# Kernel optimization log

Hardware: AMD Instinct MI355X
Metric: run time of the kernel (lower is better)

The kernel has to match this reference:

```python
import jax, jax.numpy as jnp
import numpy as np

RELU_SCALE = 0.25  # const power-of-two activation scale for QuantReLU (uint4)
DN = ('NCHW', 'OIHW', 'NCHW')
BN_EPS = 1e-5


def ste_round(x):
    # straight-through-estimator round (brevitas RoundSte)
    return x + jax.lax.stop_gradient(jnp.round(x) - x)


def fq_signed(x, bits):
    # per-tensor symmetric fixed-point fake quant with power-of-two scale
    # (Int8WeightPerTensorFixedPoint / Int8ActPerTensorFixedPoint at bit_width=bits)
    n = 2.0 ** (bits - 1) - 1.0
    m = jnp.maximum(jnp.max(jnp.abs(x)), 1e-8)
    s = jax.lax.stop_gradient(jnp.exp2(jnp.ceil(jnp.log2(m / n))))
    return jnp.clip(ste_round(x / s), -n - 1.0, n) * s


def quant_relu4(x):
    # QuantReLU: uint4, CONST power-of-two scale
    return jnp.clip(ste_round(x / RELU_SCALE), 0.0, 15.0) * RELU_SCALE


def bn(x, g, b, m, v):
    # inference-form BatchNorm2d (running stats)
    inv = g * jax.lax.rsqrt(v + BN_EPS)
    return x * inv[None, :, None, None] + (b - m * inv)[None, :, None, None]


def qconv(x, w, stride, groups):
    # QuantConv2d: fake-quant input (int4) and weight (int4), then conv
    xq = fq_signed(x, 4)
    wq = fq_signed(w, 4)
    pad = 'VALID' if w.shape[-1] == 1 else ((1, 1), (1, 1))
    return jax.lax.conv_general_dilated(
        xq, wq, (stride, stride), pad,
        dimension_numbers=DN, feature_group_count=groups)


def setup_inputs() -> dict:
    key = jax.random.key(0)
    ks = jax.random.split(key, 24)
    B, Cin, H, W = 32, 64, 56, 56
    expansion, Cout = 6, 96
    P = expansion * Cin  # 384

    def bn_params(i, C):
        g = jax.random.uniform(ks[i], (C,), minval=0.5, maxval=1.5)
        b = jax.random.normal(ks[i + 1], (C,)) * 0.1
        m = jax.random.normal(ks[i + 2], (C,)) * 0.1
        v = jax.random.uniform(ks[i + 3], (C,), minval=0.5, maxval=1.5)
        return g, b, m, v

    x = jax.random.normal(ks[0], (B, Cin, H, W), dtype=jnp.float32)
    w1 = jax.random.normal(ks[1], (P, Cin, 1, 1), dtype=jnp.float32) * 0.1
    w2 = jax.random.normal(ks[2], (P, 1, 3, 3), dtype=jnp.float32) * 0.1
    w3 = jax.random.normal(ks[3], (Cout, P, 1, 1), dtype=jnp.float32) * 0.1
    ws = jax.random.normal(ks[4], (Cout, Cin, 1, 1), dtype=jnp.float32) * 0.1
    g1, b1, m1, v1 = bn_params(5, P)
    g2, b2, m2, v2 = bn_params(9, P)
    g3, b3, m3, v3 = bn_params(13, Cout)
    gs, bs, ms, vs = bn_params(17, Cout)
    return {
        'x': x,
        'w1': w1, 'g1': g1, 'b1': b1, 'm1': m1, 'v1': v1,
        'w2': w2, 'g2': g2, 'b2': b2, 'm2': m2, 'v2': v2,
        'w3': w3, 'g3': g3, 'b3': b3, 'm3': m3, 'v3': v3,
        'ws': ws, 'gs': gs, 'bs': bs, 'ms': ms, 'vs': vs,
    }


def reference(x, w1, g1, b1, m1, v1, w2, g2, b2, m2, v2,
              w3, g3, b3, m3, v3, ws, gs, bs, ms, vs):
    P = w1.shape[0]
    # expand 1x1 -> BN -> QuantReLU
    out = quant_relu4(bn(qconv(x, w1, 1, 1), g1, b1, m1, v1))
    # depthwise 3x3 (stride=1) -> BN -> QuantReLU
    out = quant_relu4(bn(qconv(out, w2, 1, P), g2, b2, m2, v2))
    # project 1x1 with int8 output_quant -> BN
    out = bn(fq_signed(qconv(out, w3, 1, 1), 8), g3, b3, m3, v3)
    # shortcut: 1x1 quant conv (int4 output_quant) -> BN  (stride==1, Cin!=Cout)
    sc = bn(fq_signed(qconv(x, ws, 1, 1), 4), gs, bs, ms, vs)
    return quant_relu4(out + sc)
```

## Files before the change

### kernel.cpp

```cpp
#include <hip/hip_runtime.h>
#include <stdint.h>

#define B_  32
#define CIN 64
#define H_  56
#define W_  56
#define HW_ 3136
#define P_  384
#define CO_ 96

__device__ __forceinline__ float pot_scale(float m, float n) {
    float q = fmaxf(m, 1e-8f) / n;
    int e; float f = frexpf(q, &e);
    return ldexpf(1.0f, (f == 0.5f) ? (e - 1) : e);
}

__device__ __forceinline__ int dot8(int a, int b, int c) {
#if __has_builtin(__builtin_amdgcn_sdot8)
    return __builtin_amdgcn_sdot8(a, b, c, false);
#else
#pragma unroll
    for (int j = 0; j < 8; j++) {
        int av = (a << (28 - 4 * j)) >> 28;
        int bv = (b << (28 - 4 * j)) >> 28;
        c += av * bv;
    }
    return c;
#endif
}

__device__ __forceinline__ int iclamp(int v, int lo, int hi) { return min(max(v, lo), hi); }

__device__ __forceinline__ unsigned build_lut(float r, int lo) {
    unsigned v = 0;
#pragma unroll
    for (int L = 0; L < 8; L++)
        v |= (unsigned)min((int)rintf(__fmul_rn((float)(lo + L), r)), 7) << (4 * L);
    return v;
}
__device__ __forceinline__ int lut1(unsigned lo, unsigned hi, int L) {
    unsigned sel = (L & 8) ? hi : lo;
    return (int)((sel >> ((L & 7) * 4)) & 7u);
}
__device__ __forceinline__ unsigned lutn4(unsigned lo, unsigned hi, unsigned v) {
    return (unsigned)lut1(lo, hi, (int)(v & 0xffu))
         | ((unsigned)lut1(lo, hi, (int)((v >> 8) & 0xffu)) << 4)
         | ((unsigned)lut1(lo, hi, (int)((v >> 16) & 0xffu)) << 8)
         | ((unsigned)lut1(lo, hi, (int)((v >> 24) & 0xffu)) << 12);
}

__device__ __forceinline__ int block_max(int v, int* red) {
    int tid = threadIdx.x;
    red[tid] = v; __syncthreads();
    for (int s = 128; s > 0; s >>= 1) {
        if (tid < s) red[tid] = max(red[tid], red[tid + s]);
        __syncthreads();
    }
    int r = red[0];
    __syncthreads();
    return r;
}

__device__ __forceinline__ int block_max192(int v, int* red) {
    int tid = threadIdx.x;
    red[tid] = v;
    if (tid < 64) red[192 + tid] = 0;
    __syncthreads();
    for (int s = 128; s > 0; s >>= 1) {
        if (tid < s) red[tid] = max(red[tid], red[tid + s]);
        __syncthreads();
    }
    int r = red[0];
    __syncthreads();
    return r;
}


__global__ __launch_bounds__(1024) void k_init_bn(
    float* sf, float* bnb,
    const float* g1, const float* b1, const float* m1, const float* v1,
    const float* g2, const float* b2, const float* m2, const float* v2,
    const float* g3, const float* b3, const float* m3, const float* v3,
    const float* gs, const float* bs, const float* ms, const float* vs)
{
    int t = threadIdx.x;
    if (t < 32) ((int*)sf)[t] = 0;
    if (t < 384) {
        float inv = __fmul_rn(g1[t], __fdiv_rn(1.0f, sqrtf(__fadd_rn(v1[t], 1e-5f))));
        bnb[t] = inv;
        bnb[384 + t] = __fsub_rn(b1[t], __fmul_rn(m1[t], inv));
    } else if (t < 768) {
        int i = t - 384;
        float inv = __fmul_rn(g2[i], __fdiv_rn(1.0f, sqrtf(__fadd_rn(v2[i], 1e-5f))));
        bnb[768 + i] = inv;
        bnb[1152 + i] = __fsub_rn(b2[i], __fmul_rn(m2[i], inv));
    } else if (t < 864) {
        int i = t - 768;
        float inv = __fmul_rn(g3[i], __fdiv_rn(1.0f, sqrtf(__fadd_rn(v3[i], 1e-5f))));
        bnb[1536 + i] = inv;
        bnb[1632 + i] = __fsub_rn(b3[i], __fmul_rn(m3[i], inv));
    } else if (t < 960) {
        int i = t - 864;
        float inv = __fmul_rn(gs[i], __fdiv_rn(1.0f, sqrtf(__fadd_rn(vs[i], 1e-5f))));
        bnb[1728 + i] = inv;
        bnb[1824 + i] = __fsub_rn(bs[i], __fmul_rn(ms[i], inv));
    }
}

#define XBLK 2044
__global__ __launch_bounds__(256) void k_maxes(
    const float* __restrict__ x, const float* __restrict__ w1,
    const float* __restrict__ w2, const float* __restrict__ w3,
    const float* __restrict__ wsc, float* sf)
{
    __shared__ int red[256];
    int tid = threadIdx.x;
    float m = 0.f;
    if (blockIdx.x < XBLK) {
        const float4* x4 = (const float4*)x;
        const int n4 = (B_ * CIN * HW_) / 4;
        for (int i = blockIdx.x * 256 + tid; i < n4; i += XBLK * 256) {
            float4 v = x4[i];
            m = fmaxf(m, fmaxf(fmaxf(fabsf(v.x), fabsf(v.y)),
                               fmaxf(fabsf(v.z), fabsf(v.w))));
        }
        int bm = block_max(__float_as_int(m), red);
        if (tid == 0) atomicMax((int*)&sf[0], bm);
    } else {
        int seg = blockIdx.x - XBLK;
        const float* p = seg == 0 ? w1 : seg == 1 ? w2 : seg == 2 ? w3 : wsc;
        int n = seg == 0 ? P_ * CIN : seg == 1 ? P_ * 9 : seg == 2 ? CO_ * P_ : CO_ * CIN;
        for (int i = tid; i < n; i += 256) m = fmaxf(m, fabsf(p[i]));
        int bm = block_max(__float_as_int(m), red);
        if (tid == 0) atomicMax((int*)&sf[1 + seg], bm);
    }
}

__global__ __launch_bounds__(256) void k_quantx(
    const float* __restrict__ x, const float* __restrict__ sf, int* __restrict__ xq4)
{
    int t = blockIdx.x * 256 + threadIdx.x;
    float rx = 1.0f / pot_scale(sf[0], 7.0f);
    int hw4 = (t % 784) * 4;
    int c8  = (t / 784) & 7;
    int b   = t / (784 * 8);
    const float* xp = x + (size_t)(b * 64 + c8 * 8) * HW_ + hw4;
    unsigned pk[4] = {0, 0, 0, 0};
#pragma unroll
    for (int j = 0; j < 8; j++) {
        float4 v = *(const float4*)(xp + (size_t)j * HW_);
        float va[4] = {v.x, v.y, v.z, v.w};
#pragma unroll
        for (int w = 0; w < 4; w++) {
            int q = iclamp((int)rintf(__fmul_rn(va[w], rx)), -8, 7);
            pk[w] |= (unsigned)(q & 0xF) << (4 * j);
        }
    }
    int4 st = make_int4((int)pk[0], (int)pk[1], (int)pk[2], (int)pk[3]);
    *(int4*)(xq4 + (size_t)(b * 8 + c8) * HW_ + hw4) = st;
}

__global__ __launch_bounds__(256) void k_quantw(
    const float* __restrict__ w1, const float* __restrict__ w2,
    const float* __restrict__ w3, const float* __restrict__ wsc,
    const float* __restrict__ sf,
    int* __restrict__ w1n, int8_t* __restrict__ w2q,
    int* __restrict__ w3n, int* __restrict__ wsn)
{
    int flat = blockIdx.x * 256 + threadIdx.x;
    if (flat < 3072) {
        int d = flat, co = d & 3, k8 = (d >> 2) & 7, g = d >> 5;
        float r = 1.0f / pot_scale(sf[1], 7.f);
        const float* src = w1 + (4 * g + co) * 64 + 8 * k8;
        unsigned pk = 0;
#pragma unroll
        for (int j = 0; j < 8; j++) {
            int q = iclamp((int)rintf(__fmul_rn(src[j], r)), -8, 7);
            pk |= (unsigned)(q & 0xF) << (4 * j);
        }
        w1n[d] = (int)pk;
    } else if (flat < 7680) {
        int d = flat - 3072, co = d & 3, k8 = (d >> 2) % 48, coq = d / 192;
        float r = 1.0f / pot_scale(sf[3], 7.f);
        const float* src = w3 + (4 * coq + co) * 384 + 8 * k8;
        unsigned pk = 0;
#pragma unroll
        for (int j = 0; j < 8; j++) {
            int q = iclamp((int)rintf(__fmul_rn(src[j], r)), -8, 7);
            pk |= (unsigned)(q & 0xF) << (4 * j);
        }
        w3n[d] = (int)pk;
    } else if (flat < 8448) {
        int d = flat - 7680, co = d & 3, k8 = (d >> 2) & 7, coq = d >> 5;
        float r = 1.0f / pot_scale(sf[4], 7.f);
        const float* src = wsc + (4 * coq + co) * 64 + 8 * k8;
        unsigned pk = 0;
#pragma unroll
        for (int j = 0; j < 8; j++) {
            int q = iclamp((int)rintf(__fmul_rn(src[j], r)), -8, 7);
            pk |= (unsigned)(q & 0xF) << (4 * j);
        }
        wsn[d] = (int)pk;
    } else if (flat < 11904) {
        int i = flat - 8448;
        float r = 1.0f / pot_scale(sf[2], 7.f);
        w2q[i] = (int8_t)iclamp((int)rintf(__fmul_rn(w2[i], r)), -8, 7);
    }
}

__global__ __launch_bounds__(192) void k_conv1(
    const int* __restrict__ xq4, const int4* __restrict__ w1n,
    const int4* __restrict__ wsn,
    const float* __restrict__ sf, const float* __restrict__ bnb,
    unsigned* __restrict__ out1p, int* si)
{
    __shared__ __align__(16) int xs[8 * W_];
    __shared__ int red[256];
    int tid = threadIdx.x;
    int b = blockIdx.x / H_, h = blockIdx.x % H_;
    for (int i = tid; i < 8 * W_; i += 192)
        xs[i] = xq4[((b * 8 + i / W_) * HW_) + h * W_ + (i % W_)];
    float sprod = __fmul_rn(pot_scale(sf[0], 7.f), pot_scale(sf[1], 7.f));
    __syncthreads();
    int g = tid % 96, half = tid / 96;
    int4 wreg[8];
    {
        const int4* wp = w1n + g * 8;
#pragma unroll
        for (int k = 0; k < 8; k++) wreg[k] = wp[k];
    }
    float4 invv = *(const float4*)&bnb[4 * g];
    float4 betv = *(const float4*)&bnb[384 + 4 * g];
    float inva[4] = {invv.x, invv.y, invv.z, invv.w};
    float beta[4] = {betv.x, betv.y, betv.z, betv.w};
    int lmax = 0;
    unsigned* dst = out1p + (size_t)(b * 96 + g) * HW_ + h * W_;
#pragma unroll
    for (int q = 0; q < 7; q++) {
        int w4 = half * 28 + q * 4;
        int acc[4][4];
#pragma unroll
        for (int c = 0; c < 4; c++)
#pragma unroll
            for (int w = 0; w < 4; w++) acc[c][w] = 0;
#pragma unroll
        for (int k = 0; k < 8; k++) {
            int4 wv = wreg[k];
            int4 xv = *(const int4*)&xs[k * W_ + w4];
            acc[0][0] = dot8(xv.x, wv.x, acc[0][0]); acc[0][1] = dot8(xv.y, wv.x, acc[0][1]);
            acc[0][2] = dot8(xv.z, wv.x, acc[0][2]); acc[0][3] = dot8(xv.w, wv.x, acc[0][3]);
            acc[1][0] = dot8(xv.x, wv.y, acc[1][0]); acc[1][1] = dot8(xv.y, wv.y, acc[1][1]);
            acc[1][2] = dot8(xv.z, wv.y, acc[1][2]); acc[1][3] = dot8(xv.w, wv.y, acc[1][3]);
            acc[2][0] = dot8(xv.x, wv.z, acc[2][0]); acc[2][1] = dot8(xv.y, wv.z, acc[2][1]);
            acc[2][2] = dot8(xv.z, wv.z, acc[2][2]); acc[2][3] = dot8(xv.w, wv.z, acc[2][3]);
            acc[3][0] = dot8(xv.x, wv.w, acc[3][0]); acc[3][1] = dot8(xv.y, wv.w, acc[3][1]);
            acc[3][2] = dot8(xv.z, wv.w, acc[3][2]); acc[3][3] = dot8(xv.w, wv.w, acc[3][3]);
        }
        uint4 ov;
        unsigned* op = (unsigned*)&ov;
#pragma unroll
        for (int w = 0; w < 4; w++) {
            unsigned pkd = 0;
#pragma unroll
            for (int c = 0; c < 4; c++) {
                float y = __fadd_rn(__fmul_rn(__fmul_rn((float)acc[c][w], sprod), inva[c]), beta[c]);
                int L = iclamp((int)rintf(__fmul_rn(y, 4.f)), 0, 15);
                lmax = max(lmax, L);
                pkd |= (unsigned)L << (8 * c);
            }
            op[w] = pkd;
        }
        *(uint4*)(dst + w4) = ov;
    }
    int bm = block_max192(lmax, red);
    if (tid == 0) atomicMax(&si[5], bm);
    int amax = 0;
    for (int qi = tid; qi < 336; qi += 192) {
        int coq = qi / 14, w4 = (qi % 14) * 4;
        int acc[4][4];
#pragma unroll
        for (int c = 0; c < 4; c++)
#pragma unroll
            for (int w = 0; w < 4; w++) acc[c][w] = 0;
        const int4* wp = wsn + coq * 8;
#pragma unroll
        for (int k = 0; k < 8; k++) {
            int4 wv = wp[k];
            int4 xv = *(const int4*)&xs[k * W_ + w4];
            acc[0][0] = dot8(xv.x, wv.x, acc[0][0]); acc[0][1] = dot8(xv.y, wv.x, acc[0][1]);
            acc[0][2] = dot8(xv.z, wv.x, acc[0][2]); acc[0][3] = dot8(xv.w, wv.x, acc[0][3]);
            acc[1][0] = dot8(xv.x, wv.y, acc[1][0]); acc[1][1] = dot8(xv.y, wv.y, acc[1][1]);
            acc[1][2] = dot8(xv.z, wv.y, acc[1][2]); acc[1][3] = dot8(xv.w, wv.y, acc[1][3]);
            acc[2][0] = dot8(xv.x, wv.z, acc[2][0]); acc[2][1] = dot8(xv.y, wv.z, acc[2][1]);
            acc[2][2] = dot8(xv.z, wv.z, acc[2][2]); acc[2][3] = dot8(xv.w, wv.z, acc[2][3]);
            acc[3][0] = dot8(xv.x, wv.w, acc[3][0]); acc[3][1] = dot8(xv.y, wv.w, acc[3][1]);
            acc[3][2] = dot8(xv.z, wv.w, acc[3][2]); acc[3][3] = dot8(xv.w, wv.w, acc[3][3]);
        }
#pragma unroll
        for (int c = 0; c < 4; c++)
            amax = max(amax, max(max(abs(acc[c][0]), abs(acc[c][1])),
                                 max(abs(acc[c][2]), abs(acc[c][3]))));
    }
    bm = block_max192(amax, red);
    if (tid == 0) atomicMax(&si[8], bm);
}

__global__ __launch_bounds__(256) void k_conv2(
    const unsigned* __restrict__ out1p, const int8_t* __restrict__ w2q,
    const float* __restrict__ sf, int* si,
    const float* __restrict__ bnb, unsigned* __restrict__ out2p)
{
    __shared__ int plane[58 * 58];
    __shared__ int red[256];
    int tid = threadIdx.x;
    int b = blockIdx.x / 96, g = blockIdx.x % 96;
    float s_a2 = pot_scale(0.25f * (float)si[5], 7.f);
    float r2 = 0.25f / s_a2;
    float sprod = __fmul_rn(s_a2, pot_scale(sf[2], 7.f));
    unsigned lutlo = build_lut(r2, 0), luthi = build_lut(r2, 8);
    const unsigned* src = out1p + (size_t)(b * 96 + g) * HW_;
    for (int i = tid; i < 58 * 58; i += 256) {
        int r = i / 58, c = i % 58;
        int pv = 0;
        if (r >= 1 && r <= 56 && c >= 1 && c <= 56) {
            unsigned v = src[(r - 1) * W_ + (c - 1)];
            pv = lut1(lutlo, luthi, (int)(v & 0xffu))
               | (lut1(lutlo, luthi, (int)((v >> 8) & 0xffu)) << 8)
               | (lut1(lutlo, luthi, (int)((v >> 16) & 0xffu)) << 16)
               | (lut1(lutlo, luthi, (int)((v >> 24) & 0xffu)) << 24);
        }
        plane[i] = pv;
    }
    int wv[4][9];
#pragma unroll
    for (int c = 0; c < 4; c++)
#pragma unroll
        for (int t = 0; t < 9; t++) wv[c][t] = (int)w2q[(4 * g + c) * 9 + t];
    float4 invv = *(const float4*)&bnb[768 + 4 * g];
    float4 betv = *(const float4*)&bnb[1152 + 4 * g];
    float inva[4] = {invv.x, invv.y, invv.z, invv.w};
    float beta[4] = {betv.x, betv.y, betv.z, betv.w};
    __syncthreads();
    int lmax = 0;
    int ow = tid & 63, seg = tid >> 6;
    if (ow < 56) {
        int oh0 = seg * 14;
        const int* pr = plane + ow;
        unsigned* dst = out2p + (size_t)(b * 96 + g) * HW_ + ow;
        int p00 = pr[oh0 * 58],       p01 = pr[oh0 * 58 + 1],       p02 = pr[oh0 * 58 + 2];
        int p10 = pr[(oh0 + 1) * 58], p11 = pr[(oh0 + 1) * 58 + 1], p12 = pr[(oh0 + 1) * 58 + 2];
#pragma unroll 2
        for (int oh = oh0; oh < oh0 + 14; oh++) {
            int p20 = pr[(oh + 2) * 58], p21 = pr[(oh + 2) * 58 + 1], p22 = pr[(oh + 2) * 58 + 2];
            unsigned pkd = 0;
#pragma unroll
            for (int c = 0; c < 4; c++) {
                int sh = 8 * c;
                int acc = ((p00 >> sh) & 0xff) * wv[c][0] + ((p01 >> sh) & 0xff) * wv[c][1]
                        + ((p02 >> sh) & 0xff) * wv[c][2] + ((p10 >> sh) & 0xff) * wv[c][3]
                        + ((p11 >> sh) & 0xff) * wv[c][4] + ((p12 >> sh) & 0xff) * wv[c][5]
                        + ((p20 >> sh) & 0xff) * wv[c][6] + ((p21 >> sh) & 0xff) * wv[c][7]
                        + ((p22 >> sh) & 0xff) * wv[c][8];
                float y = __fadd_rn(__fmul_rn(__fmul_rn((float)acc, sprod), inva[c]), beta[c]);
                int L = iclamp((int)rintf(__fmul_rn(y, 4.f)), 0, 15);
                lmax = max(lmax, L);
                pkd |= (unsigned)L << sh;
            }
            dst[oh * W_] = pkd;
            p00 = p10; p01 = p11; p02 = p12;
            p10 = p20; p11 = p21; p12 = p22;
        }
    }
    int bm = block_max(lmax, red);
    if (tid == 0) atomicMax(&si[6], bm);
}

__global__ __launch_bounds__(256) void k_conv3(
    const unsigned* __restrict__ out2p, const int4* __restrict__ w3n,
    const float* __restrict__ sf, int* si,
    int16_t* __restrict__ acc3)
{
    __shared__ __align__(16) int a3s[2 * 48 * W_];
    __shared__ int red[256];
    int tid = threadIdx.x;
    int b = blockIdx.x / 28, h0 = (blockIdx.x % 28) * 2;
    float s_a3 = pot_scale(0.25f * (float)si[6], 7.f);
    float r3 = 0.25f / s_a3;
    unsigned lutlo = build_lut(r3, 0), luthi = build_lut(r3, 8);
    for (int i = tid; i < 2 * 48 * W_; i += 256) {
        int row = i / (48 * W_), rem = i % (48 * W_), c8 = rem / W_, w = rem % W_;
        size_t base = (size_t)(b * 96 + c8 * 2) * HW_ + (h0 + row) * W_ + w;
        unsigned v0 = out2p[base], v1 = out2p[base + HW_];
        a3s[i] = (int)(lutn4(lutlo, luthi, v0) | (lutn4(lutlo, luthi, v1) << 16));
    }
    __syncthreads();
    int amax = 0;
    for (int qi = tid; qi < 672; qi += 256) {
        int coq = qi / 28, rem2 = qi % 28, row = rem2 / 14, w4 = (rem2 % 14) * 4;
        int acc[4][4];
#pragma unroll
        for (int c = 0; c < 4; c++)
#pragma unroll
            for (int w = 0; w < 4; w++) acc[c][w] = 0;
        const int4* wp = w3n + coq * 48;
        const int* ap = a3s + row * 48 * W_ + w4;
#pragma unroll 6
        for (int k = 0; k < 48; k++) {
            int4 wv = wp[k];
            int4 av = *(const int4*)(ap + k * W_);
            acc[0][0] = dot8(av.x, wv.x, acc[0][0]); acc[0][1] = dot8(av.y, wv.x, acc[0][1]);
            acc[0][2] = dot8(av.z, wv.x, acc[0][2]); acc[0][3] = dot8(av.w, wv.x, acc[0][3]);
            acc[1][0] = dot8(av.x, wv.y, acc[1][0]); acc[1][1] = dot8(av.y, wv.y, acc[1][1]);
            acc[1][2] = dot8(av.z, wv.y, acc[1][2]); acc[1][3] = dot8(av.w, wv.y, acc[1][3]);
            acc[2][0] = dot8(av.x, wv.z, acc[2][0]); acc[2][1] = dot8(av.y, wv.z, acc[2][1]);
            acc[2][2] = dot8(av.z, wv.z, acc[2][2]); acc[2][3] = dot8(av.w, wv.z, acc[2][3]);
            acc[3][0] = dot8(av.x, wv.w, acc[3][0]); acc[3][1] = dot8(av.y, wv.w, acc[3][1]);
            acc[3][2] = dot8(av.z, wv.w, acc[3][2]); acc[3][3] = dot8(av.w, wv.w, acc[3][3]);
        }
#pragma unroll
        for (int c = 0; c < 4; c++) {
            int co = coq * 4 + c;
            amax = max(amax, max(max(abs(acc[c][0]), abs(acc[c][1])),
                                 max(abs(acc[c][2]), abs(acc[c][3]))));
            short4 st = make_short4((short)acc[c][0], (short)acc[c][1],
                                    (short)acc[c][2], (short)acc[c][3]);
            *(short4*)(acc3 + (size_t)(b * CO_ + co) * HW_ + (h0 + row) * W_ + w4) = st;
        }
    }
    int bm = block_max(amax, red);
    if (tid == 0) atomicMax(&si[7], bm);
}

__global__ __launch_bounds__(256) void k_final(
    const int* __restrict__ xq4, const int4* __restrict__ wsn,
    const int16_t* __restrict__ acc3, const float* __restrict__ sf,
    const int* __restrict__ si, const float* __restrict__ bnb,
    float* __restrict__ dout)
{
    __shared__ __align__(16) int xs[8 * W_];
    int tid = threadIdx.x;
    int b = blockIdx.x / H_, h = blockIdx.x % H_;
    for (int i = tid; i < 8 * W_; i += 256)
        xs[i] = xq4[((b * 8 + i / W_) * HW_) + h * W_ + (i % W_)];
    float s_a3   = pot_scale(0.25f * (float)si[6], 7.f);
    float sprod3 = __fmul_rn(s_a3, pot_scale(sf[3], 7.f));
    float s_q3   = pot_scale(__fmul_rn(sprod3, (float)si[7]), 127.f);
    float rq3    = sprod3 / s_q3;
    float sprods = __fmul_rn(pot_scale(sf[0], 7.f), pot_scale(sf[4], 7.f));
    float s_qs   = pot_scale(__fmul_rn(sprods, (float)si[8]), 7.f);
    float rqs    = sprods / s_qs;
    __syncthreads();
    for (int qi = tid; qi < 24 * 14; qi += 256) {
        int coq = qi / 14, w4 = (qi % 14) * 4;
        int acc[4][4];
#pragma unroll
        for (int c = 0; c < 4; c++)
#pragma unroll
            for (int w = 0; w < 4; w++) acc[c][w] = 0;
        const int4* wp = wsn + coq * 8;
#pragma unroll
        for (int k = 0; k < 8; k++) {
            int4 wv = wp[k];
            int4 xv = *(const int4*)&xs[k * W_ + w4];
            acc[0][0] = dot8(xv.x, wv.x, acc[0][0]); acc[0][1] = dot8(xv.y, wv.x, acc[0][1]);
            acc[0][2] = dot8(xv.z, wv.x, acc[0][2]); acc[0][3] = dot8(xv.w, wv.x, acc[0][3]);
            acc[1][0] = dot8(xv.x, wv.y, acc[1][0]); acc[1][1] = dot8(xv.y, wv.y, acc[1][1]);
            acc[1][2] = dot8(xv.z, wv.y, acc[1][2]); acc[1][3] = dot8(xv.w, wv.y, acc[1][3]);
            acc[2][0] = dot8(xv.x, wv.z, acc[2][0]); acc[2][1] = dot8(xv.y, wv.z, acc[2][1]);
            acc[2][2] = dot8(xv.z, wv.z, acc[2][2]); acc[2][3] = dot8(xv.w, wv.z, acc[2][3]);
            acc[3][0] = dot8(xv.x, wv.w, acc[3][0]); acc[3][1] = dot8(xv.y, wv.w, acc[3][1]);
            acc[3][2] = dot8(xv.z, wv.w, acc[3][2]); acc[3][3] = dot8(xv.w, wv.w, acc[3][3]);
        }
        float4 inv3v = *(const float4*)&bnb[1536 + 4 * coq];
        float4 bet3v = *(const float4*)&bnb[1632 + 4 * coq];
        float4 invSv = *(const float4*)&bnb[1728 + 4 * coq];
        float4 betSv = *(const float4*)&bnb[1824 + 4 * coq];
        float inv3a[4] = {inv3v.x, inv3v.y, inv3v.z, inv3v.w};
        float bet3a[4] = {bet3v.x, bet3v.y, bet3v.z, bet3v.w};
        float invSa[4] = {invSv.x, invSv.y, invSv.z, invSv.w};
        float betSa[4] = {betSv.x, betSv.y, betSv.z, betSv.w};
#pragma unroll
        for (int c = 0; c < 4; c++) {
            int co = coq * 4 + c;
            size_t idx = (size_t)(b * CO_ + co) * HW_ + h * W_ + w4;
            short4 c3 = *(const short4*)(acc3 + idx);
            int c3a[4] = {c3.x, c3.y, c3.z, c3.w};
            float4 o4;
            float* o = (float*)&o4;
#pragma unroll
            for (int j = 0; j < 4; j++) {
                int q3 = iclamp((int)rintf(__fmul_rn((float)c3a[j], rq3)), -128, 127);
                float y3 = __fadd_rn(__fmul_rn(__fmul_rn((float)q3, s_q3), inv3a[c]), bet3a[c]);
                int qs = iclamp((int)rintf(__fmul_rn((float)acc[c][j], rqs)), -8, 7);
                float ys = __fadd_rn(__fmul_rn(__fmul_rn((float)qs, s_qs), invSa[c]), betSa[c]);
                float oo = __fadd_rn(y3, ys);
                int L = iclamp((int)rintf(__fmul_rn(oo, 4.f)), 0, 15);
                o[j] = (float)L * 0.25f;
            }
            *(float4*)(dout + idx) = o4;
        }
    }
}

extern "C" void kernel_launch(void* const* d_in, const int* in_sizes, int n_in,
                              void* d_out, int out_size, void* d_ws, size_t ws_size,
                              hipStream_t stream)
{
    const float* x   = (const float*)d_in[0];
    const float* w1  = (const float*)d_in[1];
    const float* g1  = (const float*)d_in[2];
    const float* b1  = (const float*)d_in[3];
    const float* m1  = (const float*)d_in[4];
    const float* v1  = (const float*)d_in[5];
    const float* w2  = (const float*)d_in[6];
    const float* g2  = (const float*)d_in[7];
    const float* b2  = (const float*)d_in[8];
    const float* m2  = (const float*)d_in[9];
    const float* v2  = (const float*)d_in[10];
    const float* w3  = (const float*)d_in[11];
    const float* g3  = (const float*)d_in[12];
    const float* b3  = (const float*)d_in[13];
    const float* m3  = (const float*)d_in[14];
    const float* v3  = (const float*)d_in[15];
    const float* wsc = (const float*)d_in[16];
    const float* gs  = (const float*)d_in[17];
    const float* bs  = (const float*)d_in[18];
    const float* ms  = (const float*)d_in[19];
    const float* vs  = (const float*)d_in[20];

    char* ws = (char*)d_ws;
    float*    sf    = (float*)ws;
    int*      si    = (int*)ws;
    float*    bnb   = (float*)(ws + 256);
    int*      w1n   = (int*)(ws + 8192);
    int8_t*   w2q   = (int8_t*)(ws + 32768);
    int*      w3n   = (int*)(ws + 36864);
    int*      wsn   = (int*)(ws + 73728);
    int*      xq4   = (int*)(ws + (1u << 20));
    unsigned* out1p = (unsigned*)(ws + (8u << 20));
    int16_t*  acc3  = (int16_t*)(ws + (8u << 20));
    unsigned* out2p = (unsigned*)(ws + (48u << 20));

    k_init_bn<<<1, 1024, 0, stream>>>(sf, bnb, g1, b1, m1, v1, g2, b2, m2, v2,
                                      g3, b3, m3, v3, gs, bs, ms, vs);
    k_maxes<<<XBLK + 4, 256, 0, stream>>>(x, w1, w2, w3, wsc, sf);
    k_quantx<<<784, 256, 0, stream>>>(x, sf, xq4);
    k_quantw<<<47, 256, 0, stream>>>(w1, w2, w3, wsc, sf, w1n, w2q, w3n, wsn);
    k_conv1<<<B_ * H_, 192, 0, stream>>>(xq4, (const int4*)w1n, (const int4*)wsn,
                                         sf, bnb, out1p, si);
    k_conv2<<<B_ * 96, 256, 0, stream>>>(out1p, w2q, sf, si, bnb, out2p);
    k_conv3<<<B_ * 28, 256, 0, stream>>>(out2p, (const int4*)w3n, sf, si, acc3);
    k_final<<<B_ * H_, 256, 0, stream>>>(xq4, (const int4*)wsn, acc3, sf, si, bnb,
                                         (float*)d_out);
}
```

Baseline: 313.9 us.

## Fuse input quantization into conv1, pack activations to 4-bit, spread max atomics

Removes the separate k_quantx pass: conv1 now quantizes x rows on the fly and writes xq4 as a side output for the final kernel. Intermediate activations out1/out2 go from one byte per 4-bit level to 16-bit nibble-packed storage, halving their write and read traffic, and conv1 stages its output in shared memory so it can store with wide coalesced writes. Block reductions switch to wave shuffles, and the global max atomics go to 16 padded slots that readers combine, to cut atomic contention. The x max scan also uses fewer blocks. The cost is that conv1 does strided float loads of x itself and every consumer reads 16 slots per max.

Measured after the change: 274.4 us. 1.14x faster.

```diff
diff --git a/kernel.cpp b/kernel.cpp
--- a/kernel.cpp
+++ b/kernel.cpp
@@ -9,6 +9,8 @@
 #define P_  384
 #define CO_ 96
 
+typedef unsigned short u16;
+
 __device__ __forceinline__ float pot_scale(float m, float n) {
     float q = fmaxf(m, 1e-8f) / n;
     int e; float f = frexpf(q, &e);
@@ -42,42 +44,34 @@
     unsigned sel = (L & 8) ? hi : lo;
     return (int)((sel >> ((L & 7) * 4)) & 7u);
 }
-__device__ __forceinline__ unsigned lutn4(unsigned lo, unsigned hi, unsigned v) {
-    return (unsigned)lut1(lo, hi, (int)(v & 0xffu))
-         | ((unsigned)lut1(lo, hi, (int)((v >> 8) & 0xffu)) << 4)
-         | ((unsigned)lut1(lo, hi, (int)((v >> 16) & 0xffu)) << 8)
-         | ((unsigned)lut1(lo, hi, (int)((v >> 24) & 0xffu)) << 12);
-}
-
-__device__ __forceinline__ int block_max(int v, int* red) {
-    int tid = threadIdx.x;
-    red[tid] = v; __syncthreads();
-    for (int s = 128; s > 0; s >>= 1) {
-        if (tid < s) red[tid] = max(red[tid], red[tid + s]);
-        __syncthreads();
-    }
-    int r = red[0];
+__device__ __forceinline__ unsigned lutn4h(unsigned lo, unsigned hi, unsigned v) {
+    return (unsigned)lut1(lo, hi, (int)(v & 0xFu))
+         | ((unsigned)lut1(lo, hi, (int)((v >> 4) & 0xFu)) << 4)
+         | ((unsigned)lut1(lo, hi, (int)((v >> 8) & 0xFu)) << 8)
+         | ((unsigned)lut1(lo, hi, (int)((v >> 12) & 0xFu)) << 12);
+}
+
+__device__ __forceinline__ int wave_max(int v) {
+#pragma unroll
+    for (int off = 32; off > 0; off >>= 1) v = max(v, __shfl_xor(v, off, 64));
+    return v;
+}
+__device__ __forceinline__ int block_max_w(int v, int* red, int slot, int nw) {
+    v = wave_max(v);
+    int wid = threadIdx.x >> 6;
+    if ((threadIdx.x & 63) == 0) red[slot * 8 + wid] = v;
     __syncthreads();
+    int r = red[slot * 8];
+#pragma unroll 4
+    for (int i = 1; i < nw; i++) r = max(r, red[slot * 8 + i]);
     return r;
 }
 
-__device__ __forceinline__ int block_max192(int v, int* red) {
-    int tid = threadIdx.x;
-    red[tid] = v;
-    if (tid < 64) red[192 + tid] = 0;
-    __syncthreads();
-    for (int s = 128; s > 0; s >>= 1) {
-        if (tid < s) red[tid] = max(red[tid], red[tid + s]);
-        __syncthreads();
-    }
-    int r = red[0];
-    __syncthreads();
-    return r;
-}
-
+#define SMAX_RD(sm, q, dst) { dst = 0; _Pragma("unroll") \
+    for (int s_ = 0; s_ < 16; s_++) dst = max(dst, (sm)[(q) * 256 + s_ * 16]); }
 
 __global__ __launch_bounds__(1024) void k_init_bn(
-    float* sf, float* bnb,
+    float* sf, int* smax, float* bnb,
     const float* g1, const float* b1, const float* m1, const float* v1,
     const float* g2, const float* b2, const float* m2, const float* v2,
     const float* g3, const float* b3, const float* m3, const float* v3,
@@ -85,6 +79,7 @@
 {
     int t = threadIdx.x;
     if (t < 32) ((int*)sf)[t] = 0;
+    smax[t] = 0;
     if (t < 384) {
         float inv = __fmul_rn(g1[t], __fdiv_rn(1.0f, sqrtf(__fadd_rn(v1[t], 1e-5f))));
         bnb[t] = inv;
@@ -107,13 +102,13 @@
     }
 }
 
-#define XBLK 2044
+#define XBLK 384
 __global__ __launch_bounds__(256) void k_maxes(
     const float* __restrict__ x, const float* __restrict__ w1,
     const float* __restrict__ w2, const float* __restrict__ w3,
     const float* __restrict__ wsc, float* sf)
 {
-    __shared__ int red[256];
+    __shared__ int red[16];
     int tid = threadIdx.x;
     float m = 0.f;
     if (blockIdx.x < XBLK) {
@@ -124,40 +119,16 @@
             m = fmaxf(m, fmaxf(fmaxf(fabsf(v.x), fabsf(v.y)),
                                fmaxf(fabsf(v.z), fabsf(v.w))));
         }
-        int bm = block_max(__float_as_int(m), red);
+        int bm = block_max_w(__float_as_int(m), red, 0, 4);
         if (tid == 0) atomicMax((int*)&sf[0], bm);
     } else {
         int seg = blockIdx.x - XBLK;
         const float* p = seg == 0 ? w1 : seg == 1 ? w2 : seg == 2 ? w3 : wsc;
         int n = seg == 0 ? P_ * CIN : seg == 1 ? P_ * 9 : seg == 2 ? CO_ * P_ : CO_ * CIN;
         for (int i = tid; i < n; i += 256) m = fmaxf(m, fabsf(p[i]));
-        int bm = block_max(__float_as_int(m), red);
+        int bm = block_max_w(__float_as_int(m), red, 0, 4);
         if (tid == 0) atomicMax((int*)&sf[1 + seg], bm);
     }
-}
-
-__global__ __launch_bounds__(256) void k_quantx(
-    const float* __restrict__ x, const float* __restrict__ sf, int* __restrict__ xq4)
-{
-    int t = blockIdx.x * 256 + threadIdx.x;
-    float rx = 1.0f / pot_scale(sf[0], 7.0f);
-    int hw4 = (t % 784) * 4;
-    int c8  = (t / 784) & 7;
-    int b   = t / (784 * 8);
-    const float* xp = x + (size_t)(b * 64 + c8 * 8) * HW_ + hw4;
-    unsigned pk[4] = {0, 0, 0, 0};
-#pragma unroll
-    for (int j = 0; j < 8; j++) {
-        float4 v = *(const float4*)(xp + (size_t)j * HW_);
-        float va[4] = {v.x, v.y, v.z, v.w};
-#pragma unroll
-        for (int w = 0; w < 4; w++) {
-            int q = iclamp((int)rintf(__fmul_rn(va[w], rx)), -8, 7);
-            pk[w] |= (unsigned)(q & 0xF) << (4 * j);
-        }
-    }
-    int4 st = make_int4((int)pk[0], (int)pk[1], (int)pk[2], (int)pk[3]);
-    *(int4*)(xq4 + (size_t)(b * 8 + c8) * HW_ + hw4) = st;
 }
 
 __global__ __launch_bounds__(256) void k_quantw(
@@ -209,17 +180,29 @@
 }
 
 __global__ __launch_bounds__(192) void k_conv1(
-    const int* __restrict__ xq4, const int4* __restrict__ w1n,
+    const float* __restrict__ x, const int4* __restrict__ w1n,
     const int4* __restrict__ wsn,
     const float* __restrict__ sf, const float* __restrict__ bnb,
-    unsigned* __restrict__ out1p, int* si)
+    u16* __restrict__ out1h, int* __restrict__ xq4, int* smax)
 {
     __shared__ __align__(16) int xs[8 * W_];
-    __shared__ int red[256];
+    __shared__ __align__(16) u16 otile[96 * W_];
+    __shared__ int red[16];
     int tid = threadIdx.x;
     int b = blockIdx.x / H_, h = blockIdx.x % H_;
-    for (int i = tid; i < 8 * W_; i += 192)
-        xs[i] = xq4[((b * 8 + i / W_) * HW_) + h * W_ + (i % W_)];
+    float rx = 1.0f / pot_scale(sf[0], 7.0f);
+    for (int i = tid; i < 8 * W_; i += 192) {
+        int c8 = i / W_, w = i % W_;
+        const float* xp = x + (size_t)(b * 64 + c8 * 8) * HW_ + h * W_ + w;
+        unsigned pk = 0;
+#pragma unroll
+        for (int j = 0; j < 8; j++) {
+            int q = iclamp((int)rintf(__fmul_rn(xp[(size_t)j * HW_], rx)), -8, 7);
+            pk |= (unsigned)(q & 0xF) << (4 * j);
+        }
+        xs[i] = (int)pk;
+        xq4[(size_t)(b * 8 + c8) * HW_ + h * W_ + w] = (int)pk;
+    }
     float sprod = __fmul_rn(pot_scale(sf[0], 7.f), pot_scale(sf[1], 7.f));
     __syncthreads();
     int g = tid % 96, half = tid / 96;
@@ -234,7 +217,6 @@
     float inva[4] = {invv.x, invv.y, invv.z, invv.w};
     float beta[4] = {betv.x, betv.y, betv.z, betv.w};
     int lmax = 0;
-    unsigned* dst = out1p + (size_t)(b * 96 + g) * HW_ + h * W_;
 #pragma unroll
     for (int q = 0; q < 7; q++) {
         int w4 = half * 28 + q * 4;
@@ -256,8 +238,7 @@
             acc[3][0] = dot8(xv.x, wv.w, acc[3][0]); acc[3][1] = dot8(xv.y, wv.w, acc[3][1]);
             acc[3][2] = dot8(xv.z, wv.w, acc[3][2]); acc[3][3] = dot8(xv.w, wv.w, acc[3][3]);
         }
-        uint4 ov;
-        unsigned* op = (unsigned*)&ov;
+        unsigned lv[4];
 #pragma unroll
         for (int w = 0; w < 4; w++) {
             unsigned pkd = 0;
@@ -266,14 +247,23 @@
                 float y = __fadd_rn(__fmul_rn(__fmul_rn((float)acc[c][w], sprod), inva[c]), beta[c]);
                 int L = iclamp((int)rintf(__fmul_rn(y, 4.f)), 0, 15);
                 lmax = max(lmax, L);
-                pkd |= (unsigned)L << (8 * c);
+                pkd |= (unsigned)L << (4 * c);
             }
-            op[w] = pkd;
-        }
-        *(uint4*)(dst + w4) = ov;
-    }
-    int bm = block_max192(lmax, red);
-    if (tid == 0) atomicMax(&si[5], bm);
+            lv[w] = pkd;
+        }
+        *(uint2*)&otile[g * W_ + w4] =
+            make_uint2(lv[0] | (lv[1] << 16), lv[2] | (lv[3] << 16));
+    }
+    __syncthreads();
+    {
+        u16* baseo = out1h + (size_t)(b * 96) * HW_ + h * W_;
+        for (int i = tid; i < 96 * 7; i += 192) {
+            int gg = i / 7, wq = (i % 7) * 8;
+            *(uint4*)(baseo + (size_t)gg * HW_ + wq) = *(uint4*)&otile[gg * W_ + wq];
+        }
+    }
+    int bm = block_max_w(lmax, red, 0, 3);
+    if (tid == 0) atomicMax(&smax[0 * 256 + (blockIdx.x & 15) * 16], bm);
     int amax = 0;
     for (int qi = tid; qi < 336; qi += 192) {
         int coq = qi / 14, w4 = (qi % 14) * 4;
@@ -301,33 +291,34 @@
             amax = max(amax, max(max(abs(acc[c][0]), abs(acc[c][1])),
                                  max(abs(acc[c][2]), abs(acc[c][3]))));
     }
-    bm = block_max192(amax, red);
-    if (tid == 0) atomicMax(&si[8], bm);
+    bm = block_max_w(amax, red, 1, 3);
+    if (tid == 0) atomicMax(&smax[3 * 256 + (blockIdx.x & 15) * 16], bm);
 }
 
 __global__ __launch_bounds__(256) void k_conv2(
-    const unsigned* __restrict__ out1p, const int8_t* __restrict__ w2q,
-    const float* __restrict__ sf, int* si,
-    const float* __restrict__ bnb, unsigned* __restrict__ out2p)
+    const u16* __restrict__ out1h, const int8_t* __restrict__ w2q,
+    const float* __restrict__ sf, int* smax,
+    const float* __restrict__ bnb, u16* __restrict__ out2h)
 {
     __shared__ int plane[58 * 58];
-    __shared__ int red[256];
+    __shared__ int red[16];
     int tid = threadIdx.x;
     int b = blockIdx.x / 96, g = blockIdx.x % 96;
-    float s_a2 = pot_scale(0.25f * (float)si[5], 7.f);
+    int mL1; SMAX_RD(smax, 0, mL1);
+    float s_a2 = pot_scale(0.25f * (float)mL1, 7.f);
     float r2 = 0.25f / s_a2;
     float sprod = __fmul_rn(s_a2, pot_scale(sf[2], 7.f));
     unsigned lutlo = build_lut(r2, 0), luthi = build_lut(r2, 8);
-    const unsigned* src = out1p + (size_t)(b * 96 + g) * HW_;
+    const u16* src = out1h + (size_t)(b * 96 + g) * HW_;
     for (int i = tid; i < 58 * 58; i += 256) {
         int r = i / 58, c = i % 58;
         int pv = 0;
         if (r >= 1 && r <= 56 && c >= 1 && c <= 56) {
             unsigned v = src[(r - 1) * W_ + (c - 1)];
-            pv = lut1(lutlo, luthi, (int)(v & 0xffu))
-               | (lut1(lutlo, luthi, (int)((v >> 8) & 0xffu)) << 8)
-               | (lut1(lutlo, luthi, (int)((v >> 16) & 0xffu)) << 16)
-               | (lut1(lutlo, luthi, (int)((v >> 24) & 0xffu)) << 24);
+            pv = lut1(lutlo, luthi, (int)(v & 0xFu))
+               | (lut1(lutlo, luthi, (int)((v >> 4) & 0xFu)) << 8)
+               | (lut1(lutlo, luthi, (int)((v >> 8) & 0xFu)) << 16)
+               | (lut1(lutlo, luthi, (int)((v >> 12) & 0xFu)) << 24);
         }
         plane[i] = pv;
     }
@@ -346,7 +337,7 @@
     if (ow < 56) {
         int oh0 = seg * 14;
         const int* pr = plane + ow;
-        unsigned* dst = out2p + (size_t)(b * 96 + g) * HW_ + ow;
+        u16* dst = out2h + (size_t)(b * 96 + g) * HW_ + ow;
         int p00 = pr[oh0 * 58],       p01 = pr[oh0 * 58 + 1],       p02 = pr[oh0 * 58 + 2];
         int p10 = pr[(oh0 + 1) * 58], p11 = pr[(oh0 + 1) * 58 + 1], p12 = pr[(oh0 + 1) * 58 + 2];
 #pragma unroll 2
@@ -364,34 +355,35 @@
                 float y = __fadd_rn(__fmul_rn(__fmul_rn((float)acc, sprod), inva[c]), beta[c]);
                 int L = iclamp((int)rintf(__fmul_rn(y, 4.f)), 0, 15);
                 lmax = max(lmax, L);
-                pkd |= (unsigned)L << sh;
+                pkd |= (unsigned)L << (4 * c);
             }
-            dst[oh * W_] = pkd;
+            dst[oh * W_] = (u16)pkd;
             p00 = p10; p01 = p11; p02 = p12;
             p10 = p20; p11 = p21; p12 = p22;
         }
     }
-    int bm = block_max(lmax, red);
-    if (tid == 0) atomicMax(&si[6], bm);
+    int bm = block_max_w(lmax, red, 0, 4);
+    if (tid == 0) atomicMax(&smax[1 * 256 + (blockIdx.x & 15) * 16], bm);
 }
 
 __global__ __launch_bounds__(256) void k_conv3(
-    const unsigned* __restrict__ out2p, const int4* __restrict__ w3n,
-    const float* __restrict__ sf, int* si,
+    const u16* __restrict__ out2h, const int4* __restrict__ w3n,
+    const float* __restrict__ sf, int* smax,
     int16_t* __restrict__ acc3)
 {
     __shared__ __align__(16) int a3s[2 * 48 * W_];
-    __shared__ int red[256];
+    __shared__ int red[16];
     int tid = threadIdx.x;
     int b = blockIdx.x / 28, h0 = (blockIdx.x % 28) * 2;
-    float s_a3 = pot_scale(0.25f * (float)si[6], 7.f);
+    int mL2; SMAX_RD(smax, 1, mL2);
+    float s_a3 = pot_scale(0.25f * (float)mL2, 7.f);
     float r3 = 0.25f / s_a3;
     unsigned lutlo = build_lut(r3, 0), luthi = build_lut(r3, 8);
     for (int i = tid; i < 2 * 48 * W_; i += 256) {
         int row = i / (48 * W_), rem = i % (48 * W_), c8 = rem / W_, w = rem % W_;
         size_t base = (size_t)(b * 96 + c8 * 2) * HW_ + (h0 + row) * W_ + w;
-        unsigned v0 = out2p[base], v1 = out2p[base + HW_];
-        a3s[i] = (int)(lutn4(lutlo, luthi, v0) | (lutn4(lutlo, luthi, v1) << 16));
+        unsigned v0 = out2h[base], v1 = out2h[base + HW_];
+        a3s[i] = (int)(lutn4h(lutlo, luthi, v0) | (lutn4h(lutlo, luthi, v1) << 16));
     }
     __syncthreads();
     int amax = 0;
@@ -427,14 +419,14 @@
             *(short4*)(acc3 + (size_t)(b * CO_ + co) * HW_ + (h0 + row) * W_ + w4) = st;
         }
     }
-    int bm = block_max(amax, red);
-    if (tid == 0) atomicMax(&si[7], bm);
+    int bm = block_max_w(amax, red, 0, 4);
+    if (tid == 0) atomicMax(&smax[2 * 256 + (blockIdx.x & 15) * 16], bm);
 }
 
 __global__ __launch_bounds__(256) void k_final(
     const int* __restrict__ xq4, const int4* __restrict__ wsn,
     const int16_t* __restrict__ acc3, const float* __restrict__ sf,
-    const int* __restrict__ si, const float* __restrict__ bnb,
+    const int* __restrict__ smax, const float* __restrict__ bnb,
     float* __restrict__ dout)
 {
     __shared__ __align__(16) int xs[8 * W_];
@@ -442,12 +434,14 @@
     int b = blockIdx.x / H_, h = blockIdx.x % H_;
     for (int i = tid; i < 8 * W_; i += 256)
         xs[i] = xq4[((b * 8 + i / W_) * HW_) + h * W_ + (i % W_)];
-    float s_a3   = pot_scale(0.25f * (float)si[6], 7.f);
+    int mL2, mA3, mAS;
+    SMAX_RD(smax, 1, mL2); SMAX_RD(smax, 2, mA3); SMAX_RD(smax, 3, mAS);
+    float s_a3   = pot_scale(0.25f * (float)mL2, 7.f);
     float sprod3 = __fmul_rn(s_a3, pot_scale(sf[3], 7.f));
-    float s_q3   = pot_scale(__fmul_rn(sprod3, (float)si[7]), 127.f);
+    float s_q3   = pot_scale(__fmul_rn(sprod3, (float)mA3), 127.f);
     float rq3    = sprod3 / s_q3;
     float sprods = __fmul_rn(pot_scale(sf[0], 7.f), pot_scale(sf[4], 7.f));
-    float s_qs   = pot_scale(__fmul_rn(sprods, (float)si[8]), 7.f);
+    float s_qs   = pot_scale(__fmul_rn(sprods, (float)mAS), 7.f);
     float rqs    = sprods / s_qs;
     __syncthreads();
     for (int qi = tid; qi < 24 * 14; qi += 256) {
@@ -529,27 +523,26 @@
     const float* vs  = (const float*)d_in[20];
 
     char* ws = (char*)d_ws;
-    float*    sf    = (float*)ws;
-    int*      si    = (int*)ws;
-    float*    bnb   = (float*)(ws + 256);
-    int*      w1n   = (int*)(ws + 8192);
-    int8_t*   w2q   = (int8_t*)(ws + 32768);
-    int*      w3n   = (int*)(ws + 36864);
-    int*      wsn   = (int*)(ws + 73728);
-    int*      xq4   = (int*)(ws + (1u << 20));
-    unsigned* out1p = (unsigned*)(ws + (8u << 20));
-    int16_t*  acc3  = (int16_t*)(ws + (8u << 20));
-    unsigned* out2p = (unsigned*)(ws + (48u << 20));
-
-    k_init_bn<<<1, 1024, 0, stream>>>(sf, bnb, g1, b1, m1, v1, g2, b2, m2, v2,
+    float*   sf    = (float*)ws;
+    float*   bnb   = (float*)(ws + 256);
+    int*     w1n   = (int*)(ws + 8192);
+    int8_t*  w2q   = (int8_t*)(ws + 32768);
+    int*     w3n   = (int*)(ws + 36864);
+    int*     wsn   = (int*)(ws + 73728);
+    int*     smax  = (int*)(ws + 102400);
+    int*     xq4   = (int*)(ws + (1u << 20));
+    u16*     out1h = (u16*)(ws + (8u << 20));
+    int16_t* acc3  = (int16_t*)(ws + (8u << 20));
+    u16*     out2h = (u16*)(ws + (48u << 20));
+
+    k_init_bn<<<1, 1024, 0, stream>>>(sf, smax, bnb, g1, b1, m1, v1, g2, b2, m2, v2,
                                       g3, b3, m3, v3, gs, bs, ms, vs);
     k_maxes<<<XBLK + 4, 256, 0, stream>>>(x, w1, w2, w3, wsc, sf);
-    k_quantx<<<784, 256, 0, stream>>>(x, sf, xq4);
     k_quantw<<<47, 256, 0, stream>>>(w1, w2, w3, wsc, sf, w1n, w2q, w3n, wsn);
-    k_conv1<<<B_ * H_, 192, 0, stream>>>(xq4, (const int4*)w1n, (const int4*)wsn,
-                                         sf, bnb, out1p, si);
-    k_conv2<<<B_ * 96, 256, 0, stream>>>(out1p, w2q, sf, si, bnb, out2p);
-    k_conv3<<<B_ * 28, 256, 0, stream>>>(out2p, (const int4*)w3n, sf, si, acc3);
-    k_final<<<B_ * H_, 256, 0, stream>>>(xq4, (const int4*)wsn, acc3, sf, si, bnb,
+    k_conv1<<<B_ * H_, 192, 0, stream>>>(x, (const int4*)w1n, (const int4*)wsn,
+                                         sf, bnb, out1h, xq4, smax);
+    k_conv2<<<B_ * 96, 256, 0, stream>>>(out1h, w2q, sf, smax, bnb, out2h);
+    k_conv3<<<B_ * 28, 256, 0, stream>>>(out2h, (const int4*)w3n, sf, smax, acc3);
+    k_final<<<B_ * H_, 256, 0, stream>>>(xq4, (const int4*)wsn, acc3, sf, smax, bnb,
                                          (float*)d_out);
 }
```
